# Kernel optimization log

Measured on AMD Instinct MI355X. Metric: run time of the kernel, lower is better.

## Reference

```python
import jax, jax.numpy as jnp
import numpy as np

N, K, D_IN, D_OUT = 50000, 32, 128, 128

def setup_inputs() -> dict:
    key = jax.random.key(0)
    ks = jax.random.split(key, 7)
    s = 1.0 / np.sqrt(D_IN)
    return {
        "self_vecs": jax.random.normal(ks[0], (N, D_IN), dtype=jnp.float32),
        "neigh_vecs": jax.random.normal(ks[1], (N, K, D_IN), dtype=jnp.float32),
        "neigh_deltatime": jax.random.uniform(ks[2], (N, K), dtype=jnp.float32),
        "W1": jax.random.normal(ks[3], (D_IN, D_OUT), dtype=jnp.float32) * s,
        "W2": jax.random.normal(ks[4], (D_IN, D_OUT), dtype=jnp.float32) * s,
        "W3": jax.random.normal(ks[5], (1, D_OUT), dtype=jnp.float32),
        "W4": jax.random.normal(ks[6], (D_OUT, 1), dtype=jnp.float32) * (1.0 / np.sqrt(D_OUT)),
        "b4": jnp.zeros((1,), dtype=jnp.float32),
    }

def reference(self_vecs, neigh_vecs, neigh_deltatime, W1, W2, W3, W4, b4):
    # self query: [N,1,Dout]
    q = (self_vecs @ W1)[:, None, :]
    # neighbor memory: [N,K,Dout]
    m = jnp.einsum('nkd,de->nke', neigh_vecs, W2)
    # delta-time memory: sigmoid(dt[...,None] @ W3) -> [N,K,Dout]
    t = jax.nn.sigmoid(neigh_deltatime[:, :, None] * W3[0])
    # additive attention score: relu((q+m+t) @ W4 + b4) -> [N,K,1]
    score = jax.nn.relu(jnp.einsum('nke,eo->nko', q + m + t, W4) + b4)
    # softmax over neighbor axis (axis=1)
    score = jax.nn.softmax(score, axis=1)
    # weighted neighbor sum: score^T @ neigh -> [N,Din]
    output = jnp.einsum('nko,nkd->nd', score, neigh_vecs)
    return output, jnp.squeeze(score, axis=-1)
```

## Files before the change

### kernel.cpp

```cpp
#include <hip/hip_runtime.h>

#define KN    32
#define DIN   128
#define TBL   2048

__global__ void precompute(const float* __restrict__ W1,
                           const float* __restrict__ W2,
                           const float* __restrict__ W3,
                           const float* __restrict__ W4,
                           const float* __restrict__ b4,
                           float* __restrict__ uv,
                           float* __restrict__ table)
{
    const int t = blockIdx.x * blockDim.x + threadIdx.x;
    if (blockIdx.x == 0) {
        const int tid = threadIdx.x;
        if (tid < DIN) {
            const float* row = W2 + tid * DIN;
            float acc = 0.f;
            for (int e = 0; e < DIN; ++e) acc += row[e] * W4[e];
            uv[tid] = acc;
        } else {
            const int d = tid - DIN;
            const float* row = W1 + d * DIN;
            float acc = 0.f;
            for (int e = 0; e < DIN; ++e) acc += row[e] * W4[e];
            uv[DIN + d] = acc;
        }
    }
    for (int i = t; i <= TBL; i += gridDim.x * blockDim.x) {
        const float x = (float)i * (1.0f / (float)TBL);
        float acc = b4[0];
        for (int e = 0; e < DIN; ++e)
            acc += W4[e] / (1.0f + __expf(-x * W3[e]));
        table[i] = acc;
    }
}

__global__ __launch_bounds__(256) void attn_agg(
    const float* __restrict__ self_vecs,
    const float* __restrict__ neigh_vecs,
    const float* __restrict__ dt,
    const float* __restrict__ uv,
    const float* __restrict__ table,
    float* __restrict__ out,
    float* __restrict__ score_out)
{
    __shared__ float s_p[KN * 33];
    __shared__ __align__(16) float s_part[8 * DIN];
    __shared__ float s_score[KN];
    __shared__ float s_qw4;

    const int n   = blockIdx.x;
    const int tid = threadIdx.x;
    const int g   = tid >> 5;
    const int q   = tid & 31;

    const float4* gsrc = (const float4*)(neigh_vecs + (size_t)n * KN * DIN);
    const float4 val0 = gsrc[tid];
    const float4 val1 = gsrc[tid + 256];
    const float4 val2 = gsrc[tid + 512];
    const float4 val3 = gsrc[tid + 768];
    const float4 u4   = *(const float4*)(uv + 4 * q);

    if (tid < 64) {
        const float* v  = uv + DIN;
        const float* sv = self_vecs + (size_t)n * DIN;
        float qp = sv[tid] * v[tid] + sv[tid + 64] * v[tid + 64];
        #pragma unroll
        for (int off = 32; off > 0; off >>= 1)
            qp += __shfl_down(qp, off, 64);
        if (tid == 0) s_qw4 = qp;
    }

    s_p[ g       * 33 + q] = val0.x*u4.x + val0.y*u4.y + val0.z*u4.z + val0.w*u4.w;
    s_p[(g +  8) * 33 + q] = val1.x*u4.x + val1.y*u4.y + val1.z*u4.z + val1.w*u4.w;
    s_p[(g + 16) * 33 + q] = val2.x*u4.x + val2.y*u4.y + val2.z*u4.z + val2.w*u4.w;
    s_p[(g + 24) * 33 + q] = val3.x*u4.x + val3.y*u4.y + val3.z*u4.z + val3.w*u4.w;
    __syncthreads();

    if (tid < 64) {
        const int k = tid & 31;
        const int h = tid >> 5;
        const float* pr = s_p + k * 33 + h * 16;
        float s = 0.f;
        #pragma unroll
        for (int j = 0; j < 16; ++j) s += pr[j];
        s += __shfl_down(s, 32, 64);
        if (tid < 32) {
            const float dtk = dt[(size_t)n * KN + k];
            float fx = fminf(fmaxf(dtk, 0.0f), 1.0f) * (float)TBL;
            int   i0 = min((int)fx, TBL - 1);
            const float fr = fx - (float)i0;
            const float t0 = table[i0];
            const float t1 = table[i0 + 1];
            float sp = s_qw4 + s + t0 + fr * (t1 - t0);
            sp = sp > 0.f ? sp : 0.f;
            float mx = sp;
            #pragma unroll
            for (int off = 16; off > 0; off >>= 1)
                mx = fmaxf(mx, __shfl_xor(mx, off, 32));
            const float ex = __expf(sp - mx);
            float sm = ex;
            #pragma unroll
            for (int off = 16; off > 0; off >>= 1)
                sm += __shfl_xor(sm, off, 32);
            const float sc = ex / sm;
            s_score[k] = sc;
            score_out[(size_t)n * KN + k] = sc;
        }
    }
    __syncthreads();

    {
        const float sc0 = s_score[g];
        const float sc1 = s_score[g + 8];
        const float sc2 = s_score[g + 16];
        const float sc3 = s_score[g + 24];
        float4 po;
        po.x = sc0*val0.x + sc1*val1.x + sc2*val2.x + sc3*val3.x;
        po.y = sc0*val0.y + sc1*val1.y + sc2*val2.y + sc3*val3.y;
        po.z = sc0*val0.z + sc1*val1.z + sc2*val2.z + sc3*val3.z;
        po.w = sc0*val0.w + sc1*val1.w + sc2*val2.w + sc3*val3.w;
        *(float4*)(s_part + g * DIN + 4 * q) = po;
    }
    __syncthreads();

    if (tid < DIN) {
        float acc = 0.f;
        #pragma unroll
        for (int gg = 0; gg < 8; ++gg) acc += s_part[gg * DIN + tid];
        out[(size_t)n * DIN + tid] = acc;
    }
}

extern "C" void kernel_launch(void* const* d_in, const int* in_sizes, int n_in,
                              void* d_out, int out_size, void* d_ws, size_t ws_size,
                              hipStream_t stream) {
    const float* self_vecs = (const float*)d_in[0];
    const float* neigh     = (const float*)d_in[1];
    const float* dtim      = (const float*)d_in[2];
    const float* W1        = (const float*)d_in[3];
    const float* W2        = (const float*)d_in[4];
    const float* W3        = (const float*)d_in[5];
    const float* W4        = (const float*)d_in[6];
    const float* b4        = (const float*)d_in[7];

    const int N = in_sizes[0] / DIN;
    float* uv    = (float*)d_ws;
    float* table = uv + 256;
    float* out       = (float*)d_out;
    float* score_out = out + (size_t)N * DIN;

    precompute<<<9, 256, 0, stream>>>(W1, W2, W3, W4, b4, uv, table);
    attn_agg<<<N, 256, 0, stream>>>(self_vecs, neigh, dtim, uv, table,
                                    out, score_out);
}
```

Before: 1.057 ms.

## Use persistent blocks with register prefetch of the next node's neighbors

The kernel now launches a fixed grid of 2048 blocks instead of one block per node, and each block loops over a contiguous range of nodes. While it computes the current node, it loads the next node's neighbor vectors, self vector and delta times into registers, so global-load latency overlaps with compute. The aim is to cut per-block launch overhead and memory stalls. The trade-offs are higher register pressure from the double-buffered float4 values, possibly lower occupancy, and a raw s_barrier macro in place of __syncthreads.

Result: slower. 1.096 ms (+3.7%).

```diff
diff --git a/kernel.cpp b/kernel.cpp
--- a/kernel.cpp
+++ b/kernel.cpp
@@ -3,6 +3,10 @@
 #define KN    32
 #define DIN   128
 #define TBL   2048
+#define GRID  2048
+
+#define BAR() do { asm volatile("s_waitcnt lgkmcnt(0)" ::: "memory"); \
+                   __builtin_amdgcn_s_barrier(); } while (0)
 
 __global__ void precompute(const float* __restrict__ W1,
                            const float* __restrict__ W2,
@@ -44,93 +48,124 @@
     const float* __restrict__ uv,
     const float* __restrict__ table,
     float* __restrict__ out,
-    float* __restrict__ score_out)
+    float* __restrict__ score_out,
+    int N, int per_blk)
 {
     __shared__ float s_p[KN * 33];
     __shared__ __align__(16) float s_part[8 * DIN];
     __shared__ float s_score[KN];
     __shared__ float s_qw4;
 
-    const int n   = blockIdx.x;
     const int tid = threadIdx.x;
     const int g   = tid >> 5;
     const int q   = tid & 31;
 
-    const float4* gsrc = (const float4*)(neigh_vecs + (size_t)n * KN * DIN);
-    const float4 val0 = gsrc[tid];
-    const float4 val1 = gsrc[tid + 256];
-    const float4 val2 = gsrc[tid + 512];
-    const float4 val3 = gsrc[tid + 768];
-    const float4 u4   = *(const float4*)(uv + 4 * q);
+    const int n0 = blockIdx.x * per_blk;
+    const int n1 = min(n0 + per_blk, N);
+    if (n0 >= n1) return;
 
+    const float4 u4 = *(const float4*)(uv + 4 * q);
+    float vl0 = 0.f, vl1 = 0.f;
+    if (tid < 64) { vl0 = uv[DIN + tid]; vl1 = uv[DIN + tid + 64]; }
+
+    const float4* gsrc = (const float4*)(neigh_vecs + (size_t)n0 * KN * DIN);
+    float4 c0 = gsrc[tid];
+    float4 c1 = gsrc[tid + 256];
+    float4 c2 = gsrc[tid + 512];
+    float4 c3 = gsrc[tid + 768];
+    float dt_c = 0.f, sv0_c = 0.f, sv1_c = 0.f;
     if (tid < 64) {
-        const float* v  = uv + DIN;
-        const float* sv = self_vecs + (size_t)n * DIN;
-        float qp = sv[tid] * v[tid] + sv[tid + 64] * v[tid + 64];
-        #pragma unroll
-        for (int off = 32; off > 0; off >>= 1)
-            qp += __shfl_down(qp, off, 64);
-        if (tid == 0) s_qw4 = qp;
+        const float* sv = self_vecs + (size_t)n0 * DIN;
+        sv0_c = sv[tid];
+        sv1_c = sv[tid + 64];
+        if (tid < 32) dt_c = dt[(size_t)n0 * KN + tid];
     }
 
-    s_p[ g       * 33 + q] = val0.x*u4.x + val0.y*u4.y + val0.z*u4.z + val0.w*u4.w;
-    s_p[(g +  8) * 33 + q] = val1.x*u4.x + val1.y*u4.y + val1.z*u4.z + val1.w*u4.w;
-    s_p[(g + 16) * 33 + q] = val2.x*u4.x + val2.y*u4.y + val2.z*u4.z + val2.w*u4.w;
-    s_p[(g + 24) * 33 + q] = val3.x*u4.x + val3.y*u4.y + val3.z*u4.z + val3.w*u4.w;
-    __syncthreads();
+    for (int n = n0; n < n1; ++n) {
+        float4 x0 = {0,0,0,0}, x1 = {0,0,0,0}, x2 = {0,0,0,0}, x3 = {0,0,0,0};
+        float dt_n = 0.f, sv0_n = 0.f, sv1_n = 0.f;
+        if (n + 1 < n1) {
+            const float4* gn = (const float4*)(neigh_vecs + (size_t)(n + 1) * KN * DIN);
+            x0 = gn[tid];
+            x1 = gn[tid + 256];
+            x2 = gn[tid + 512];
+            x3 = gn[tid + 768];
+            if (tid < 64) {
+                const float* svn = self_vecs + (size_t)(n + 1) * DIN;
+                sv0_n = svn[tid];
+                sv1_n = svn[tid + 64];
+                if (tid < 32) dt_n = dt[(size_t)(n + 1) * KN + tid];
+            }
+        }
 
-    if (tid < 64) {
-        const int k = tid & 31;
-        const int h = tid >> 5;
-        const float* pr = s_p + k * 33 + h * 16;
-        float s = 0.f;
-        #pragma unroll
-        for (int j = 0; j < 16; ++j) s += pr[j];
-        s += __shfl_down(s, 32, 64);
-        if (tid < 32) {
-            const float dtk = dt[(size_t)n * KN + k];
-            float fx = fminf(fmaxf(dtk, 0.0f), 1.0f) * (float)TBL;
-            int   i0 = min((int)fx, TBL - 1);
-            const float fr = fx - (float)i0;
-            const float t0 = table[i0];
-            const float t1 = table[i0 + 1];
-            float sp = s_qw4 + s + t0 + fr * (t1 - t0);
-            sp = sp > 0.f ? sp : 0.f;
-            float mx = sp;
+        if (tid < 64) {
+            float qp = sv0_c * vl0 + sv1_c * vl1;
             #pragma unroll
-            for (int off = 16; off > 0; off >>= 1)
-                mx = fmaxf(mx, __shfl_xor(mx, off, 32));
-            const float ex = __expf(sp - mx);
-            float sm = ex;
+            for (int off = 32; off > 0; off >>= 1)
+                qp += __shfl_down(qp, off, 64);
+            if (tid == 0) s_qw4 = qp;
+        }
+        s_p[ g       * 33 + q] = c0.x*u4.x + c0.y*u4.y + c0.z*u4.z + c0.w*u4.w;
+        s_p[(g +  8) * 33 + q] = c1.x*u4.x + c1.y*u4.y + c1.z*u4.z + c1.w*u4.w;
+        s_p[(g + 16) * 33 + q] = c2.x*u4.x + c2.y*u4.y + c2.z*u4.z + c2.w*u4.w;
+        s_p[(g + 24) * 33 + q] = c3.x*u4.x + c3.y*u4.y + c3.z*u4.z + c3.w*u4.w;
+        BAR();
+
+        if (tid < 64) {
+            const int k = tid & 31;
+            const int h = tid >> 5;
+            const float* pr = s_p + k * 33 + h * 16;
+            float s = 0.f;
             #pragma unroll
-            for (int off = 16; off > 0; off >>= 1)
-                sm += __shfl_xor(sm, off, 32);
-            const float sc = ex / sm;
-            s_score[k] = sc;
-            score_out[(size_t)n * KN + k] = sc;
+            for (int j = 0; j < 16; ++j) s += pr[j];
+            s += __shfl_down(s, 32, 64);
+            if (tid < 32) {
+                float fx = fminf(fmaxf(dt_c, 0.0f), 1.0f) * (float)TBL;
+                int   i0 = min((int)fx, TBL - 1);
+                const float fr = fx - (float)i0;
+                const float t0 = table[i0];
+                const float t1 = table[i0 + 1];
+                float sp = s_qw4 + s + t0 + fr * (t1 - t0);
+                sp = sp > 0.f ? sp : 0.f;
+                float mx = sp;
+                #pragma unroll
+                for (int off = 16; off > 0; off >>= 1)
+                    mx = fmaxf(mx, __shfl_xor(mx, off, 32));
+                const float ex = __expf(sp - mx);
+                float sm = ex;
+                #pragma unroll
+                for (int off = 16; off > 0; off >>= 1)
+                    sm += __shfl_xor(sm, off, 32);
+                const float sc = ex / sm;
+                s_score[k] = sc;
+                score_out[(size_t)n * KN + k] = sc;
+            }
         }
-    }
-    __syncthreads();
+        BAR();
 
-    {
-        const float sc0 = s_score[g];
-        const float sc1 = s_score[g + 8];
-        const float sc2 = s_score[g + 16];
-        const float sc3 = s_score[g + 24];
-        float4 po;
-        po.x = sc0*val0.x + sc1*val1.x + sc2*val2.x + sc3*val3.x;
-        po.y = sc0*val0.y + sc1*val1.y + sc2*val2.y + sc3*val3.y;
-        po.z = sc0*val0.z + sc1*val1.z + sc2*val2.z + sc3*val3.z;
-        po.w = sc0*val0.w + sc1*val1.w + sc2*val2.w + sc3*val3.w;
-        *(float4*)(s_part + g * DIN + 4 * q) = po;
-    }
-    __syncthreads();
+        {
+            const float sc0 = s_score[g];
+            const float sc1 = s_score[g + 8];
+            const float sc2 = s_score[g + 16];
+            const float sc3 = s_score[g + 24];
+            float4 po;
+            po.x = sc0*c0.x + sc1*c1.x + sc2*c2.x + sc3*c3.x;
+            po.y = sc0*c0.y + sc1*c1.y + sc2*c2.y + sc3*c3.y;
+            po.z = sc0*c0.z + sc1*c1.z + sc2*c2.z + sc3*c3.z;
+            po.w = sc0*c0.w + sc1*c1.w + sc2*c2.w + sc3*c3.w;
+            *(float4*)(s_part + g * DIN + 4 * q) = po;
+        }
+        BAR();
 
-    if (tid < DIN) {
-        float acc = 0.f;
-        #pragma unroll
-        for (int gg = 0; gg < 8; ++gg) acc += s_part[gg * DIN + tid];
-        out[(size_t)n * DIN + tid] = acc;
+        if (tid < DIN) {
+            float acc = 0.f;
+            #pragma unroll
+            for (int gg = 0; gg < 8; ++gg) acc += s_part[gg * DIN + tid];
+            out[(size_t)n * DIN + tid] = acc;
+        }
+
+        c0 = x0; c1 = x1; c2 = x2; c3 = x3;
+        dt_c = dt_n; sv0_c = sv0_n; sv1_c = sv1_n;
     }
 }
 
@@ -152,7 +187,9 @@
     float* out       = (float*)d_out;
     float* score_out = out + (size_t)N * DIN;
 
+    const int per_blk = (N + GRID - 1) / GRID;
+
     precompute<<<9, 256, 0, stream>>>(W1, W2, W3, W4, b4, uv, table);
-    attn_agg<<<N, 256, 0, stream>>>(self_vecs, neigh, dtim, uv, table,
-                                    out, score_out);
+    attn_agg<<<GRID, 256, 0, stream>>>(self_vecs, neigh, dtim, uv, table,
+                                       out, score_out, N, per_blk);
 }
```
